# Performance work log

Measured on AMD Instinct MI355X. Metric: run time of the kernel, lower is better.

The kernel has to match this reference:

```python
import jax, jax.numpy as jnp
import numpy as np
from jax import lax

BS, H, W, NA = 128, 64, 64, 4
C1, C2, HID = 16, 32, 512

def setup_inputs() -> dict:
    key = jax.random.key(0)
    ks = jax.random.split(key, 12)
    s = 0.05
    return {
        "diffs": jax.random.uniform(ks[0], (BS, NA, 2), jnp.float32) * 4.0,  # agent locations
        "states": jax.random.normal(ks[1], (BS, NA * 3, H, W), jnp.float32),
        "conv1_w": jax.random.normal(ks[2], (C1, 3, 8, 8), jnp.float32) * s,
        "conv1_b": jnp.zeros((C1,), jnp.float32),
        "conv2_w": jax.random.normal(ks[3], (C2, C1, 5, 5), jnp.float32) * s,
        "conv2_b": jnp.zeros((C2,), jnp.float32),
        "g_w": jax.random.normal(ks[4], (HID, 2 * C2 + 2), jnp.float32) * s,
        "g_b": jnp.zeros((HID,), jnp.float32),
        "fc4_w": jax.random.normal(ks[5], (2, HID), jnp.float32) * s,
        "fc4_b": jnp.zeros((2,), jnp.float32),
        "fc5_w": jax.random.normal(ks[6], (1, HID), jnp.float32) * s,
        "fc5_b": jnp.zeros((1,), jnp.float32),
    }

def _conv(x, w, b):
    y = lax.conv_general_dilated(x, w, (1, 1), 'VALID',
                                 dimension_numbers=('NCHW', 'OIHW', 'NCHW'))
    return jax.nn.relu(y + b[None, :, None, None])

def reference(diffs, states, conv1_w, conv1_b, conv2_w, conv2_b,
              g_w, g_b, fc4_w, fc4_b, fc5_w, fc5_b):
    bs = states.shape[0]
    # ---- encoder: per-agent CNN + global max pool ----
    x = states.reshape(bs * NA, 3, H, W)
    x = _conv(x, conv1_w, conv1_b)
    x = _conv(x, conv2_w, conv2_b)
    feat = jnp.max(x, axis=(2, 3)).reshape(bs, NA, C2)  # (bs, 4, 32)
    # ---- coordinator: adjacency from pairwise location diffs ----
    locs = diffs
    pdiffs = locs[:, :, None, :] - locs[:, None, :, :]  # (bs, 4, 4, 2)
    norms = jnp.linalg.norm(pdiffs, axis=-1)
    thresh = jnp.linalg.norm(jnp.array([1.0, 1.0], jnp.float32))
    A = (norms < thresh).astype(jnp.float32)
    A = A / jnp.clip(jnp.sum(A, axis=-1, keepdims=True), 1e-6)  # row-normalized adjacency
    mask = 1.0 - jnp.eye(NA, dtype=jnp.float32)  # messages skip j == i
    Am = A * mask  # (bs, 4, 4)
    # ---- CatEdgeGraphLayer: h_i = relu(W [f_i ; sum_j A_ij [f_j ; d_ij]] + b) ----
    feat_agg = jnp.einsum('bij,bjc->bic', Am, feat)          # (bs, 4, 32)
    diff_agg = jnp.einsum('bij,bijd->bid', Am, pdiffs)       # (bs, 4, 2)
    h = jnp.concatenate([feat, feat_agg, diff_agg], axis=-1)  # (bs, 4, 66)
    h = jax.nn.relu(jnp.einsum('bic,oc->bio', h, g_w) + g_b)  # (bs, 4, 512)
    policies = jnp.einsum('bic,oc->bio', h, fc4_w) + fc4_b    # (bs, 4, 2)
    values = jnp.einsum('bic,oc->bio', h, fc5_w) + fc5_b      # (bs, 4, 1)
    return (policies, values)
```

## Files before the change

### kernel.cpp

```cpp
#include <hip/hip_runtime.h>
#include <hip/hip_bf16.h>

#define H1 57
#define H2 53
#define XP 60

typedef _Float16 f16;
typedef _Float16 f16x4 __attribute__((ext_vector_type(4)));
typedef _Float16 f16x8 __attribute__((ext_vector_type(8)));
typedef float f32x4 __attribute__((ext_vector_type(4)));

__global__ __launch_bounds__(256) void k_repack(const float* __restrict__ w1,
    const float* __restrict__ w2, const float* __restrict__ gw,
    f16* __restrict__ w1f, f16* __restrict__ w2f,
    float2* __restrict__ gwT2, float* __restrict__ feat)
{
  const int tid = blockIdx.x * 256 + threadIdx.x;
  const int stride = 32 * 256;
  for (int i = tid; i < 8 * 64 * 8; i += stride) {
    int j = i & 7;
    int l = (i >> 3) & 63;
    int tp = i >> 9;
    int c = j & 3;
    int kw = 4 * (j >> 2) + (l >> 4);
    int oc = l & 15;
    float v = (c < 3) ? w1[((oc * 3 + c) * 8 + tp) * 8 + kw] : 0.f;
    w1f[i] = (f16)v;
  }
  for (int i = tid; i < 13 * 2 * 64 * 8; i += stride) {
    int j = i & 7;
    int l = (i >> 3) & 63;
    int h = (i >> 9) & 1;
    int tp = i >> 10;
    int tap = 2 * tp + (j >> 2);
    int c = ((l >> 4) << 2) + (j & 3);
    int oc = (l & 15) + (h << 4);
    float v = (tap < 25) ? w2[((oc * 16 + c) * 5 + tap / 5) * 5 + tap % 5] : 0.f;
    w2f[i] = (f16)v;
  }
  for (int i = tid; i < 66 * 256; i += stride) {
    int t = i & 255;
    int c = i >> 8;
    float2 v;
    v.x = gw[(2 * t) * 66 + c];
    v.y = gw[(2 * t + 1) * 66 + c];
    gwT2[i] = v;
  }
  for (int i = tid; i < 512 * 32; i += stride) feat[i] = 0.f;
}

__global__ __launch_bounds__(256) void k_conv1(const float* __restrict__ in,
    const f16* __restrict__ w1f, const float* __restrict__ b1,
    f16* __restrict__ O1)
{
  __shared__ __align__(16) f16 sIn[15][72][4];
  __shared__ __align__(16) f16 sT[4][64][20];
  const int img = blockIdx.x;
  const int y0 = min((int)blockIdx.y * 8, 49);
  const int lane = threadIdx.x & 63;
  const int wv = threadIdx.x >> 6;

  f16x8 Bf[8];
  #pragma unroll
  for (int tp = 0; tp < 8; ++tp)
    Bf[tp] = *(const f16x8*)&w1f[(tp * 64 + lane) * 8];

  for (int i = threadIdx.x; i < 15 * 16; i += 256) {
    int y = i >> 4, xq = i & 15;
    const float* p0 = &in[(((size_t)img * 3 + 0) * 64 + (y0 + y)) * 64 + xq * 4];
    float4 v0 = *(const float4*)p0;
    float4 v1 = *(const float4*)(p0 + 4096);
    float4 v2 = *(const float4*)(p0 + 8192);
    float c0[4] = {v0.x, v0.y, v0.z, v0.w};
    float c1[4] = {v1.x, v1.y, v1.z, v1.w};
    float c2[4] = {v2.x, v2.y, v2.z, v2.w};
    #pragma unroll
    for (int q = 0; q < 4; ++q) {
      f16x4 tt = {(f16)c0[q], (f16)c1[q], (f16)c2[q], (f16)0.f};
      *(f16x4*)&sIn[y][xq * 4 + q][0] = tt;
    }
  }
  for (int i = threadIdx.x; i < 15 * 8; i += 256) {
    int y = i >> 3, xi = i & 7;
    *(f16x4*)&sIn[y][64 + xi][0] = (f16x4){(f16)0.f, (f16)0.f, (f16)0.f, (f16)0.f};
  }
  __syncthreads();

  const int g = lane >> 4;
  const int n16 = lane & 15;

  const float bias = b1[n16];
  f32x4 acc[2][4];
  #pragma unroll
  for (int r = 0; r < 2; ++r)
    #pragma unroll
    for (int xt = 0; xt < 4; ++xt)
      acc[r][xt] = (f32x4){bias, bias, bias, bias};

  #pragma unroll
  for (int tp = 0; tp < 8; ++tp) {
    #pragma unroll
    for (int r = 0; r < 2; ++r) {
      const int row = 2 * wv + r + tp;
      #pragma unroll
      for (int xt = 0; xt < 4; ++xt) {
        const int px = xt * 16 + n16;
        f16x4 a0 = *(const f16x4*)&sIn[row][px + g][0];
        f16x4 a1 = *(const f16x4*)&sIn[row][px + 4 + g][0];
        union { struct { f16x4 lo, hi; } pr; f16x8 v; } u;
        u.pr.lo = a0; u.pr.hi = a1;
        acc[r][xt] = __builtin_amdgcn_mfma_f32_16x16x32_f16(u.v, Bf[tp], acc[r][xt], 0, 0, 0);
      }
    }
  }

  #pragma unroll
  for (int r = 0; r < 2; ++r) {
    #pragma unroll
    for (int xt = 0; xt < 4; ++xt)
      #pragma unroll
      for (int q = 0; q < 4; ++q)
        sT[wv][xt * 16 + g * 4 + q][n16] = (f16)fmaxf(acc[r][xt][q], 0.f);
    const int yy = y0 + 2 * wv + r;
    if (lane < H1) {
      #pragma unroll
      for (int go = 0; go < 4; ++go) {
        f16x4 v = *(const f16x4*)&sT[wv][lane][go * 4];
        *(f16x4*)&O1[(((size_t)(img * 4 + go) * H1 + yy) * XP + lane) * 4] = v;
      }
    }
  }
}

__global__ __launch_bounds__(256) void k_conv2(const f16* __restrict__ O1,
    const f16* __restrict__ w2f, const float* __restrict__ b2,
    float* __restrict__ feat)
{
  __shared__ __align__(16) f16 sW[13 * 2 * 64 * 8];
  __shared__ __align__(16) f16 sI[4 * 12 * XP * 4 + 64];
  __shared__ unsigned smax[32];
  const int img = blockIdx.x;
  const int y0 = min((int)blockIdx.y * 8, 45);
  if (threadIdx.x < 32) smax[threadIdx.x] = 0u;
  for (int i = threadIdx.x; i < 1664; i += 256)
    ((float4*)sW)[i] = ((const float4*)w2f)[i];
  for (int i = threadIdx.x; i < 4 * 360; i += 256) {
    int gg = i / 360, r = i % 360;
    ((float4*)sI)[gg * 360 + r] =
        *(const float4*)(O1 + (((size_t)(img * 4 + gg) * H1 + y0) * XP) * 4 + r * 8);
  }
  __syncthreads();

  const int lane = threadIdx.x & 63;
  const int wv = threadIdx.x >> 6;
  const int g = lane >> 4;
  const int n16 = lane & 15;

  f32x4 acc[2][4][2];
  #pragma unroll
  for (int r = 0; r < 2; ++r)
    #pragma unroll
    for (int xt = 0; xt < 4; ++xt)
      #pragma unroll
      for (int h = 0; h < 2; ++h)
        acc[r][xt][h] = (f32x4){0.f, 0.f, 0.f, 0.f};

  for (int tp = 0; tp < 13; ++tp) {
    f16x8 B0 = *(const f16x8*)&sW[((tp * 2 + 0) * 64 + lane) * 8];
    f16x8 B1 = *(const f16x8*)&sW[((tp * 2 + 1) * 64 + lane) * 8];
    const int t0 = 2 * tp;
    const int t1c = (t0 + 1 < 25) ? t0 + 1 : 0;
    const int kh0 = t0 / 5, kw0 = t0 % 5;
    const int kh1 = t1c / 5, kw1 = t1c % 5;
    #pragma unroll
    for (int r = 0; r < 2; ++r) {
      const int yl = 2 * wv + r;
      const int row0 = (g * 12 + yl + kh0) * XP;
      const int row1 = (g * 12 + yl + kh1) * XP;
      #pragma unroll
      for (int xt = 0; xt < 4; ++xt) {
        const int px = xt * 16 + n16;
        f16x4 a0 = *(const f16x4*)&sI[(row0 + px + kw0) * 4];
        f16x4 a1 = *(const f16x4*)&sI[(row1 + px + kw1) * 4];
        union { struct { f16x4 lo, hi; } pr; f16x8 v; } u;
        u.pr.lo = a0; u.pr.hi = a1;
        acc[r][xt][0] = __builtin_amdgcn_mfma_f32_16x16x32_f16(u.v, B0, acc[r][xt][0], 0, 0, 0);
        acc[r][xt][1] = __builtin_amdgcn_mfma_f32_16x16x32_f16(u.v, B1, acc[r][xt][1], 0, 0, 0);
      }
    }
  }

  const float bias0 = b2[n16];
  const float bias1 = b2[n16 + 16];
  float m0 = 0.f, m1 = 0.f;
  #pragma unroll
  for (int r = 0; r < 2; ++r)
    #pragma unroll
    for (int xt = 0; xt < 4; ++xt)
      #pragma unroll
      for (int q = 0; q < 4; ++q) {
        int px = xt * 16 + g * 4 + q;
        if (px < H2) {
          m0 = fmaxf(m0, acc[r][xt][0][q] + bias0);
          m1 = fmaxf(m1, acc[r][xt][1][q] + bias1);
        }
      }
  m0 = fmaxf(m0, 0.f);
  m1 = fmaxf(m1, 0.f);
  m0 = fmaxf(m0, __shfl_xor(m0, 16, 64));
  m0 = fmaxf(m0, __shfl_xor(m0, 32, 64));
  m1 = fmaxf(m1, __shfl_xor(m1, 16, 64));
  m1 = fmaxf(m1, __shfl_xor(m1, 32, 64));
  if (g == 0) {
    atomicMax(&smax[n16], __float_as_uint(m0));
    atomicMax(&smax[n16 + 16], __float_as_uint(m1));
  }
  __syncthreads();
  if (threadIdx.x < 32)
    atomicMax((unsigned*)&feat[img * 32 + threadIdx.x], smax[threadIdx.x]);
}

__global__ __launch_bounds__(256) void k_head(const float* __restrict__ diffs,
    const float* __restrict__ feat, const float2* __restrict__ gwT2,
    const float* __restrict__ gb, const float* __restrict__ w4,
    const float* __restrict__ b4, const float* __restrict__ w5,
    const float* __restrict__ b5, float* __restrict__ out)
{
  __shared__ float h66[4][66];
  __shared__ float hout[4][512];
  __shared__ float Am[4][4];
  __shared__ float pd[4][4][2];
  __shared__ float fs[4][32];
  const int b = blockIdx.x;
  const int tid = threadIdx.x;
  if (tid < 128) {
    int i = tid >> 5, c = tid & 31;
    fs[i][c] = feat[(b * 4 + i) * 32 + c];
  }
  if (tid == 0) {
    float lx[4], ly[4];
    #pragma unroll
    for (int a = 0; a < 4; ++a) {
      lx[a] = diffs[(b * 4 + a) * 2];
      ly[a] = diffs[(b * 4 + a) * 2 + 1];
    }
    #pragma unroll
    for (int i = 0; i < 4; ++i) {
      float A[4];
      float rs = 0.f;
      #pragma unroll
      for (int j = 0; j < 4; ++j) {
        float dx = lx[i] - lx[j], dy = ly[i] - ly[j];
        pd[i][j][0] = dx;
        pd[i][j][1] = dy;
        float n = sqrtf(dx * dx + dy * dy);
        A[j] = (n < 1.41421356237309504880f) ? 1.f : 0.f;
        rs += A[j];
      }
      float inv = 1.f / fmaxf(rs, 1e-6f);
      #pragma unroll
      for (int j = 0; j < 4; ++j)
        Am[i][j] = (i == j) ? 0.f : A[j] * inv;
    }
  }
  __syncthreads();
  if (tid < 128) {
    int i = tid >> 5, c = tid & 31;
    h66[i][c] = fs[i][c];
    float s = 0.f;
    #pragma unroll
    for (int j = 0; j < 4; ++j) s += Am[i][j] * fs[j][c];
    h66[i][32 + c] = s;
  } else if (tid < 136) {
    int q = tid - 128;
    int i = q >> 1, d = q & 1;
    float s = 0.f;
    #pragma unroll
    for (int j = 0; j < 4; ++j) s += Am[i][j] * pd[i][j][d];
    h66[i][64 + d] = s;
  }
  __syncthreads();
  {
    const float b0 = gb[2 * tid], b1g = gb[2 * tid + 1];
    float a[4][2];
    #pragma unroll
    for (int i = 0; i < 4; ++i) { a[i][0] = b0; a[i][1] = b1g; }
    #pragma unroll 6
    for (int c = 0; c < 66; ++c) {
      float2 w = gwT2[c * 256 + tid];
      #pragma unroll
      for (int i = 0; i < 4; ++i) {
        float h = h66[i][c];
        a[i][0] = fmaf(h, w.x, a[i][0]);
        a[i][1] = fmaf(h, w.y, a[i][1]);
      }
    }
    #pragma unroll
    for (int i = 0; i < 4; ++i) {
      float2 v;
      v.x = fmaxf(a[i][0], 0.f);
      v.y = fmaxf(a[i][1], 0.f);
      *(float2*)&hout[i][2 * tid] = v;
    }
  }
  __syncthreads();
  if (tid < 192) {
    int gq = tid >> 4, l = tid & 15;
    int i = gq / 3, k = gq % 3;
    const float* wrow = (k < 2) ? &w4[k * 512] : w5;
    float s = 0.f;
    for (int o = l; o < 512; o += 16) s = fmaf(hout[i][o], wrow[o], s);
    #pragma unroll
    for (int d = 8; d >= 1; d >>= 1) s += __shfl_xor(s, d, 16);
    if (l == 0) {
      if (k < 2) out[(b * 4 + i) * 2 + k] = s + b4[k];
      else       out[1024 + b * 4 + i] = s + b5[0];
    }
  }
}

extern "C" void kernel_launch(void* const* d_in, const int* in_sizes, int n_in,
                              void* d_out, int out_size, void* d_ws, size_t ws_size,
                              hipStream_t stream) {
  const float* diffs  = (const float*)d_in[0];
  const float* states = (const float*)d_in[1];
  const float* w1 = (const float*)d_in[2];
  const float* b1 = (const float*)d_in[3];
  const float* w2 = (const float*)d_in[4];
  const float* b2 = (const float*)d_in[5];
  const float* gw = (const float*)d_in[6];
  const float* gb = (const float*)d_in[7];
  const float* w4 = (const float*)d_in[8];
  const float* b4 = (const float*)d_in[9];
  const float* w5 = (const float*)d_in[10];
  const float* b5 = (const float*)d_in[11];
  float* out = (float*)d_out;

  char* base = (char*)d_ws;
  f16*    w1f  = (f16*)base;
  f16*    w2f  = (f16*)(base + 8192);
  float2* gwT2 = (float2*)(base + 34816);
  float*  feat = (float*)(base + 169984);
  f16*    O1   = (f16*)(base + 235520);

  k_repack<<<32, 256, 0, stream>>>(w1, w2, gw, w1f, w2f, gwT2, feat);
  k_conv1<<<dim3(512, 8), 256, 0, stream>>>(states, w1f, b1, O1);
  k_conv2<<<dim3(512, 7), 256, 0, stream>>>(O1, w2f, b2, feat);
  k_head<<<128, 256, 0, stream>>>(diffs, feat, gwT2, gb, w4, b4, w5, b5, out);
}
```

Baseline: 99.71 us.

## Switch conv2 to 32x32x16 MFMA with 16-channel interleaved activation layout

Conv1 output is stored channel-interleaved (16 f16 per pixel) instead of four planes of 4 channels, and the conv2 weights are repacked per tap for 32 output channels by 16 input channels. Conv2 now issues one 32x32x16 MFMA per tap per row/half instead of padded tap-pairs on 16x16x32, removing the zero-padded 26th tap and reducing the number of MFMA and LDS-load instructions. Bias is folded into the accumulator init. The larger accumulators raise register pressure, and the new layout changes LDS bank access patterns.

```diff
diff --git a/kernel.cpp b/kernel.cpp
--- a/kernel.cpp
+++ b/kernel.cpp
@@ -9,6 +9,7 @@
 typedef _Float16 f16x4 __attribute__((ext_vector_type(4)));
 typedef _Float16 f16x8 __attribute__((ext_vector_type(8)));
 typedef float f32x4 __attribute__((ext_vector_type(4)));
+typedef float f32x16 __attribute__((ext_vector_type(16)));
 
 __global__ __launch_bounds__(256) void k_repack(const float* __restrict__ w1,
     const float* __restrict__ w2, const float* __restrict__ gw,
@@ -27,16 +28,13 @@
     float v = (c < 3) ? w1[((oc * 3 + c) * 8 + tp) * 8 + kw] : 0.f;
     w1f[i] = (f16)v;
   }
-  for (int i = tid; i < 13 * 2 * 64 * 8; i += stride) {
+  for (int i = tid; i < 25 * 64 * 8; i += stride) {
     int j = i & 7;
     int l = (i >> 3) & 63;
-    int h = (i >> 9) & 1;
-    int tp = i >> 10;
-    int tap = 2 * tp + (j >> 2);
-    int c = ((l >> 4) << 2) + (j & 3);
-    int oc = (l & 15) + (h << 4);
-    float v = (tap < 25) ? w2[((oc * 16 + c) * 5 + tap / 5) * 5 + tap % 5] : 0.f;
-    w2f[i] = (f16)v;
+    int tap = i >> 9;
+    int oc = l & 31;
+    int ch = ((l >> 5) << 3) + j;
+    w2f[i] = (f16)w2[((oc * 16 + ch) * 5 + tap / 5) * 5 + tap % 5];
   }
   for (int i = tid; i < 66 * 256; i += stride) {
     int t = i & 255;
@@ -123,11 +121,16 @@
         sT[wv][xt * 16 + g * 4 + q][n16] = (f16)fmaxf(acc[r][xt][q], 0.f);
     const int yy = y0 + 2 * wv + r;
     if (lane < H1) {
-      #pragma unroll
-      for (int go = 0; go < 4; ++go) {
-        f16x4 v = *(const f16x4*)&sT[wv][lane][go * 4];
-        *(f16x4*)&O1[(((size_t)(img * 4 + go) * H1 + yy) * XP + lane) * 4] = v;
-      }
+      f16x4 v0 = *(const f16x4*)&sT[wv][lane][0];
+      f16x4 v1 = *(const f16x4*)&sT[wv][lane][4];
+      f16x4 v2 = *(const f16x4*)&sT[wv][lane][8];
+      f16x4 v3 = *(const f16x4*)&sT[wv][lane][12];
+      union { struct { f16x4 a, b; } pr; f16x8 v; } lo, hi;
+      lo.pr.a = v0; lo.pr.b = v1;
+      hi.pr.a = v2; hi.pr.b = v3;
+      f16* dst = &O1[(((size_t)img * H1 + yy) * XP + lane) * 16];
+      *(f16x8*)dst = lo.v;
+      *(f16x8*)(dst + 8) = hi.v;
     }
   }
 }
@@ -136,85 +139,75 @@
     const f16* __restrict__ w2f, const float* __restrict__ b2,
     float* __restrict__ feat)
 {
-  __shared__ __align__(16) f16 sW[13 * 2 * 64 * 8];
-  __shared__ __align__(16) f16 sI[4 * 12 * XP * 4 + 64];
+  __shared__ __align__(16) f16 sW[25 * 64 * 8];
+  __shared__ __align__(16) f16 sI[12 * 2 * 60 * 8 + 64];
   __shared__ unsigned smax[32];
   const int img = blockIdx.x;
   const int y0 = min((int)blockIdx.y * 8, 45);
   if (threadIdx.x < 32) smax[threadIdx.x] = 0u;
-  for (int i = threadIdx.x; i < 1664; i += 256)
+  for (int i = threadIdx.x; i < 1600; i += 256)
     ((float4*)sW)[i] = ((const float4*)w2f)[i];
-  for (int i = threadIdx.x; i < 4 * 360; i += 256) {
-    int gg = i / 360, r = i % 360;
-    ((float4*)sI)[gg * 360 + r] =
-        *(const float4*)(O1 + (((size_t)(img * 4 + gg) * H1 + y0) * XP) * 4 + r * 8);
+  for (int i = threadIdx.x; i < 1440; i += 256) {
+    int y = i / 120;
+    int rem = i - y * 120;
+    int oct = rem / 60;
+    int x = rem - oct * 60;
+    ((float4*)sI)[i] =
+        *(const float4*)(O1 + (((size_t)img * H1 + y0 + y) * XP + x) * 16 + oct * 8);
   }
   __syncthreads();
 
   const int lane = threadIdx.x & 63;
   const int wv = threadIdx.x >> 6;
-  const int g = lane >> 4;
-  const int n16 = lane & 15;
-
-  f32x4 acc[2][4][2];
+  const int m32 = lane & 31;
+  const int G = lane >> 5;
+
+  const float bias = b2[m32];
+  f32x16 acc[2][2];
   #pragma unroll
   for (int r = 0; r < 2; ++r)
     #pragma unroll
-    for (int xt = 0; xt < 4; ++xt)
-      #pragma unroll
-      for (int h = 0; h < 2; ++h)
-        acc[r][xt][h] = (f32x4){0.f, 0.f, 0.f, 0.f};
-
-  for (int tp = 0; tp < 13; ++tp) {
-    f16x8 B0 = *(const f16x8*)&sW[((tp * 2 + 0) * 64 + lane) * 8];
-    f16x8 B1 = *(const f16x8*)&sW[((tp * 2 + 1) * 64 + lane) * 8];
-    const int t0 = 2 * tp;
-    const int t1c = (t0 + 1 < 25) ? t0 + 1 : 0;
-    const int kh0 = t0 / 5, kw0 = t0 % 5;
-    const int kh1 = t1c / 5, kw1 = t1c % 5;
-    #pragma unroll
-    for (int r = 0; r < 2; ++r) {
-      const int yl = 2 * wv + r;
-      const int row0 = (g * 12 + yl + kh0) * XP;
-      const int row1 = (g * 12 + yl + kh1) * XP;
-      #pragma unroll
-      for (int xt = 0; xt < 4; ++xt) {
-        const int px = xt * 16 + n16;
-        f16x4 a0 = *(const f16x4*)&sI[(row0 + px + kw0) * 4];
-        f16x4 a1 = *(const f16x4*)&sI[(row1 + px + kw1) * 4];
-        union { struct { f16x4 lo, hi; } pr; f16x8 v; } u;
-        u.pr.lo = a0; u.pr.hi = a1;
-        acc[r][xt][0] = __builtin_amdgcn_mfma_f32_16x16x32_f16(u.v, B0, acc[r][xt][0], 0, 0, 0);
-        acc[r][xt][1] = __builtin_amdgcn_mfma_f32_16x16x32_f16(u.v, B1, acc[r][xt][1], 0, 0, 0);
-      }
-    }
-  }
-
-  const float bias0 = b2[n16];
-  const float bias1 = b2[n16 + 16];
-  float m0 = 0.f, m1 = 0.f;
+    for (int h = 0; h < 2; ++h)
+      #pragma unroll
+      for (int q = 0; q < 16; ++q)
+        acc[r][h][q] = bias;
+
+  const f16* pA[2][2];
   #pragma unroll
   for (int r = 0; r < 2; ++r)
     #pragma unroll
-    for (int xt = 0; xt < 4; ++xt)
-      #pragma unroll
-      for (int q = 0; q < 4; ++q) {
-        int px = xt * 16 + g * 4 + q;
-        if (px < H2) {
-          m0 = fmaxf(m0, acc[r][xt][0][q] + bias0);
-          m1 = fmaxf(m1, acc[r][xt][1][q] + bias1);
-        }
-      }
-  m0 = fmaxf(m0, 0.f);
-  m1 = fmaxf(m1, 0.f);
-  m0 = fmaxf(m0, __shfl_xor(m0, 16, 64));
-  m0 = fmaxf(m0, __shfl_xor(m0, 32, 64));
-  m1 = fmaxf(m1, __shfl_xor(m1, 16, 64));
-  m1 = fmaxf(m1, __shfl_xor(m1, 32, 64));
-  if (g == 0) {
-    atomicMax(&smax[n16], __float_as_uint(m0));
-    atomicMax(&smax[n16 + 16], __float_as_uint(m1));
-  }
+    for (int h = 0; h < 2; ++h)
+      pA[r][h] = &sI[(((2 * wv + r) * 2 + G) * XP + h * 32 + m32) * 8];
+  const f16* pB = &sW[lane * 8];
+
+  #pragma unroll
+  for (int tap = 0; tap < 25; ++tap) {
+    const int kh = tap / 5, kw = tap % 5;
+    const int off = (kh * 2 * XP + kw) * 8;
+    f16x8 Bv = *(const f16x8*)(pB + tap * 512);
+    #pragma unroll
+    for (int r = 0; r < 2; ++r)
+      #pragma unroll
+      for (int h = 0; h < 2; ++h) {
+        f16x8 Av = *(const f16x8*)(pA[r][h] + off);
+        acc[r][h] = __builtin_amdgcn_mfma_f32_32x32x16_f16(Av, Bv, acc[r][h], 0, 0, 0);
+      }
+  }
+
+  float m = 0.f;
+  #pragma unroll
+  for (int r = 0; r < 2; ++r)
+    #pragma unroll
+    for (int h = 0; h < 2; ++h)
+      #pragma unroll
+      for (int q = 0; q < 16; ++q) {
+        int row = (q & 3) + 8 * (q >> 2) + 4 * G;
+        int px = h * 32 + row;
+        if (px < H2) m = fmaxf(m, acc[r][h][q]);
+      }
+  m = fmaxf(m, 0.f);
+  m = fmaxf(m, __shfl_xor(m, 32, 64));
+  if (lane < 32) atomicMax(&smax[m32], __float_as_uint(m));
   __syncthreads();
   if (threadIdx.x < 32)
     atomicMax((unsigned*)&feat[img * 32 + threadIdx.x], smax[threadIdx.x]);
```

Measured after the change: 94.37 us. 5.4% less time.
